# Optimization experiments

Hardware: AMD Instinct MI355X
Metric: run time of the kernel (lower is better)

The kernel has to match this reference:

```python
import jax, jax.numpy as jnp
import numpy as np

H = 1024          # hiddenSize
V = 50257         # outputSize (vocab)
L = 512           # maxLength (encoder length)


def setup_inputs() -> dict:
    key = jax.random.key(0)
    ks = jax.random.split(key, 16)
    s = 0.02
    return {
        "input": jax.random.randint(ks[0], (1,), 0, V),
        "hidden": jax.random.normal(ks[1], (1, 1, H), jnp.float32),
        "encoder_outputs": jax.random.normal(ks[2], (L, H), jnp.float32),
        "emb": jax.random.normal(ks[3], (V, H), jnp.float32) * s,
        "W_attn": jax.random.normal(ks[4], (L, 2 * H), jnp.float32) * s,
        "b_attn": jnp.zeros((L,), jnp.float32),
        "W_comb": jax.random.normal(ks[5], (H, 2 * H), jnp.float32) * s,
        "b_comb": jnp.zeros((H,), jnp.float32),
        "W_ih": jax.random.normal(ks[6], (3 * H, H), jnp.float32) * s,
        "W_hh": jax.random.normal(ks[7], (3 * H, H), jnp.float32) * s,
        "b_ih": jnp.zeros((3 * H,), jnp.float32),
        "b_hh": jnp.zeros((3 * H,), jnp.float32),
        "W_out": jax.random.normal(ks[8], (V, H), jnp.float32) * s,
        "b_out": jnp.zeros((V,), jnp.float32),
    }


def reference(input, hidden, encoder_outputs, emb, W_attn, b_attn,
              W_comb, b_comb, W_ih, W_hh, b_ih, b_hh, W_out, b_out):
    # embedding lookup: [1, H] (dropout p=0 -> identity)
    embedded = emb[input]
    h = hidden[0]                                   # [1, H]
    # attention over encoder positions
    attn_logits = jnp.concatenate([embedded, h], axis=1) @ W_attn.T + b_attn
    attn_weights = jax.nn.softmax(attn_logits, axis=1)      # [1, L]
    attn_applied = attn_weights @ encoder_outputs           # [1, H]
    # combine and relu
    x = jnp.concatenate([embedded, attn_applied], axis=1) @ W_comb.T + b_comb
    x = jax.nn.relu(x)                                      # [1, H]
    # single GRU step (PyTorch gate layout: r, z, n)
    gi = x @ W_ih.T + b_ih                                  # [1, 3H]
    gh = h @ W_hh.T + b_hh                                  # [1, 3H]
    i_r, i_z, i_n = jnp.split(gi, 3, axis=1)
    h_r, h_z, h_n = jnp.split(gh, 3, axis=1)
    r = jax.nn.sigmoid(i_r + h_r)
    z = jax.nn.sigmoid(i_z + h_z)
    n = jnp.tanh(i_n + r * h_n)
    h_new = (1.0 - z) * n + z * h                           # [1, H]
    # output distribution
    output = jax.nn.log_softmax(h_new @ W_out.T + b_out, axis=1)  # [1, V]
    return output, h_new[None], attn_weights
```

## Files before the change

kernel.cpp:

```cpp
#include <hip/hip_runtime.h>
#include <cmath>

#define H 1024
#define V 50257
#define L 512
#define NB5 1571
#define NPART 128

typedef float f4 __attribute__((ext_vector_type(4)));

__device__ __forceinline__ float wred_sum(float v) {
#pragma unroll
    for (int o = 32; o > 0; o >>= 1) v += __shfl_xor(v, o, 64);
    return v;
}
__device__ __forceinline__ float dot4f(f4 a, f4 b) {
    return a.x * b.x + a.y * b.y + a.z * b.z + a.w * b.w;
}
__device__ __forceinline__ void ms_merge(float& m, float& s, float m2, float s2) {
    float M = fmaxf(m, m2);
    if (M == -INFINITY) { m = M; s = 0.f; return; }
    s = s * expf(m - M) + s2 * expf(m2 - M);
    m = M;
}

__global__ void k_phase1(const int* __restrict__ tok,
                         const float* __restrict__ hid,
                         const float* __restrict__ emb,
                         const float* __restrict__ Wa,
                         const float* __restrict__ ba,
                         const float* __restrict__ enc,
                         const float* __restrict__ Whh,
                         const float* __restrict__ bhh,
                         float* __restrict__ elg,
                         float* __restrict__ pbuf,
                         float* __restrict__ gh) {
    const int t = threadIdx.x, lane = t & 63, wv = t >> 6, b = blockIdx.x;
    const f4* h4 = (const f4*)hid;
    if (b < NPART) {
        const int l = b * 4 + wv;
        const f4* e4 = (const f4*)(emb + (size_t)tok[0] * H);
        const f4* wr = (const f4*)(Wa + (size_t)l * 2048);
        float acc = 0.f;
#pragma unroll
        for (int k = 0; k < 8; ++k) {
            int f = 64 * k + lane;
            f4 s = (f < 256) ? e4[f] : h4[f - 256];
            acc += dot4f(wr[f], s);
        }
        acc = wred_sum(acc);
        __shared__ float se[4];
        const float e = expf(acc + ba[l]);
        if (lane == 0) { se[wv] = e; elg[l] = e; }
        __syncthreads();
        f4 a = {0.f, 0.f, 0.f, 0.f};
#pragma unroll
        for (int r = 0; r < 4; ++r)
            a += se[r] * ((const f4*)(enc + (size_t)(b * 4 + r) * H))[t];
        ((f4*)pbuf)[b * 256 + t] = a;
    } else {
        const int j = (b - NPART) * 4 + wv;
        const f4* wh = (const f4*)(Whh + (size_t)j * H);
        float acc = 0.f;
#pragma unroll
        for (int k = 0; k < 4; ++k) {
            int f = 64 * k + lane;
            acc += dot4f(wh[f], h4[f]);
        }
        acc = wred_sum(acc);
        if (lane == 0) gh[j] = acc + bhh[j];
    }
}

__global__ void k_reduce(const float* __restrict__ elg,
                         const float* __restrict__ pbuf,
                         float* __restrict__ aa,
                         float* __restrict__ wout) {
    const int t = threadIdx.x, b = blockIdx.x;
    const int g = t >> 6, c = t & 63;
    __shared__ float red[4];
    const float e0 = elg[t], e1 = elg[t + 256];
    float s = wred_sum(e0 + e1);
    if (c == 0) red[g] = s;
    __syncthreads();
    const float invS = 1.f / (red[0] + red[1] + red[2] + red[3]);
    const int col = b * 64 + c;
    f4 a = {0.f, 0.f, 0.f, 0.f};
#pragma unroll 8
    for (int i = g; i < NPART; i += 4) a += ((const f4*)pbuf)[i * 256 + col];
    __shared__ f4 racc[4][64];
    racc[g][c] = a;
    __syncthreads();
    if (g == 0) {
        f4 tot = (racc[0][c] + racc[1][c] + racc[2][c] + racc[3][c]) * invS;
        ((f4*)aa)[col] = tot;
    }
    if (b == 0) { wout[t] = e0 * invS; wout[t + 256] = e1 * invS; }
}

__global__ void k_comb(const int* __restrict__ tok,
                       const float* __restrict__ emb,
                       const float* __restrict__ aa,
                       const float* __restrict__ Wc,
                       const float* __restrict__ bcb,
                       float* __restrict__ xv) {
    const int lane = threadIdx.x & 63, wv = threadIdx.x >> 6;
    const int j = blockIdx.x * 4 + wv;
    const f4* e4 = (const f4*)(emb + (size_t)tok[0] * H);
    const f4* a4 = (const f4*)aa;
    const f4* wr = (const f4*)(Wc + (size_t)j * 2048);
    float acc = 0.f;
#pragma unroll
    for (int k = 0; k < 4; ++k) {
        int f = 64 * k + lane;
        acc += dot4f(wr[f], e4[f]);
        acc += dot4f(wr[256 + f], a4[f]);
    }
    acc = wred_sum(acc);
    if (lane == 0) xv[j] = fmaxf(acc + bcb[j], 0.f);
}

__global__ void k_gates_gru(const float* __restrict__ xv,
                            const float* __restrict__ hid,
                            const float* __restrict__ Wih,
                            const float* __restrict__ bih,
                            const float* __restrict__ gh,
                            float* __restrict__ hn_out,
                            float* __restrict__ hn_ws) {
    const int lane = threadIdx.x & 63, wv = threadIdx.x >> 6;
    const int j = blockIdx.x * 4 + wv;
    const f4* x4 = (const f4*)xv;
    f4 xreg[4];
#pragma unroll
    for (int k = 0; k < 4; ++k) xreg[k] = x4[64 * k + lane];
    float g[3];
#pragma unroll
    for (int p = 0; p < 3; ++p) {
        const f4* wr = (const f4*)(Wih + (size_t)(j + p * H) * H);
        float acc = 0.f;
#pragma unroll
        for (int k = 0; k < 4; ++k) acc += dot4f(wr[64 * k + lane], xreg[k]);
        g[p] = wred_sum(acc) + bih[j + p * H];
    }
    if (lane == 0) {
        float r = 1.f / (1.f + expf(-(g[0] + gh[j])));
        float z = 1.f / (1.f + expf(-(g[1] + gh[j + H])));
        float n = tanhf(g[2] + r * gh[j + 2 * H]);
        float hv = (1.f - z) * n + z * hid[j];
        hn_out[j] = hv;
        hn_ws[j] = hv;
    }
}

__global__ void k_out_gemv(const float* __restrict__ hn,
                           const float* __restrict__ Wo,
                           const float* __restrict__ bo,
                           float* __restrict__ logits,
                           float* __restrict__ pm,
                           float* __restrict__ ps) {
    const int lane = threadIdx.x & 63, wv = threadIdx.x >> 6;
    const int b = blockIdx.x;
    const int rbase = b * 32 + wv * 8;
    const f4* h4 = (const f4*)hn;
    f4 hreg[4];
#pragma unroll
    for (int k = 0; k < 4; ++k) hreg[k] = h4[64 * k + lane];
    float m = -INFINITY, s = 0.f;
    if (b != NB5 - 1) {
        float lv[8];
#pragma unroll
        for (int i = 0; i < 8; ++i) {
            const f4* wr = (const f4*)(Wo + (size_t)(rbase + i) * H);
            float acc = 0.f;
#pragma unroll
            for (int k = 0; k < 4; ++k)
                acc += dot4f(__builtin_nontemporal_load(wr + 64 * k + lane), hreg[k]);
            acc = wred_sum(acc) + bo[rbase + i];
            if (lane == 0) logits[rbase + i] = acc;
            lv[i] = acc;
        }
#pragma unroll
        for (int i = 0; i < 8; ++i) m = fmaxf(m, lv[i]);
#pragma unroll
        for (int i = 0; i < 8; ++i) s += expf(lv[i] - m);
    } else {
#pragma unroll
        for (int i = 0; i < 8; ++i) {
            const int v = rbase + i;
            if (v < V) {
                const f4* wr = (const f4*)(Wo + (size_t)v * H);
                float acc = 0.f;
#pragma unroll
                for (int k = 0; k < 4; ++k)
                    acc += dot4f(__builtin_nontemporal_load(wr + 64 * k + lane), hreg[k]);
                acc = wred_sum(acc) + bo[v];
                if (lane == 0) logits[v] = acc;
                float M = fmaxf(m, acc);
                s = s * expf(m - M) + expf(acc - M);
                m = M;
            }
        }
    }
    __shared__ float smm[4], sms[4];
    if (lane == 0) { smm[wv] = m; sms[wv] = s; }
    __syncthreads();
    if (threadIdx.x == 0) {
        float M = smm[0], S = sms[0];
#pragma unroll
        for (int i = 1; i < 4; ++i) ms_merge(M, S, smm[i], sms[i]);
        pm[b] = M; ps[b] = S;
    }
}

__global__ void k_finalize(float* __restrict__ out,
                           const float* __restrict__ pm,
                           const float* __restrict__ ps) {
    const int t = threadIdx.x, lane = t & 63, wv = t >> 6;
    float m = -INFINITY, s = 0.f;
    for (int i = t; i < NB5; i += 256) ms_merge(m, s, pm[i], ps[i]);
#pragma unroll
    for (int o = 32; o > 0; o >>= 1) {
        float m2 = __shfl_xor(m, o, 64);
        float s2 = __shfl_xor(s, o, 64);
        ms_merge(m, s, m2, s2);
    }
    __shared__ float smm[4], sms[4];
    __shared__ float Cs;
    if (lane == 0) { smm[wv] = m; sms[wv] = s; }
    __syncthreads();
    if (t == 0) {
        float M = smm[0], S = sms[0];
#pragma unroll
        for (int i = 1; i < 4; ++i) ms_merge(M, S, smm[i], sms[i]);
        Cs = M + logf(S);
    }
    __syncthreads();
    const float C = Cs;
    const int v = blockIdx.x * 256 + t;
    if (v < V) out[v] -= C;
}

extern "C" void kernel_launch(void* const* d_in, const int* in_sizes, int n_in,
                              void* d_out, int out_size, void* d_ws, size_t ws_size,
                              hipStream_t stream) {
    const int*   tok = (const int*)d_in[0];
    const float* hid = (const float*)d_in[1];
    const float* enc = (const float*)d_in[2];
    const float* emb = (const float*)d_in[3];
    const float* Wa  = (const float*)d_in[4];
    const float* ba  = (const float*)d_in[5];
    const float* Wc  = (const float*)d_in[6];
    const float* bc  = (const float*)d_in[7];
    const float* Wih = (const float*)d_in[8];
    const float* Whh = (const float*)d_in[9];
    const float* bih = (const float*)d_in[10];
    const float* bhh = (const float*)d_in[11];
    const float* Wo  = (const float*)d_in[12];
    const float* bo  = (const float*)d_in[13];

    float* out = (float*)d_out;
    float* ws  = (float*)d_ws;
    float* elg  = ws;
    float* gh   = ws + 512;
    float* aa   = ws + 3584;
    float* xv   = ws + 4608;
    float* hn   = ws + 5632;
    float* pm   = ws + 6656;
    float* psum = ws + 8256;
    float* pbuf = ws + 9856;

    float* out_logits = out;
    float* out_hnew   = out + V;
    float* out_attnw  = out + V + H;

    k_phase1<<<NPART + 768, 256, 0, stream>>>(tok, hid, emb, Wa, ba, enc, Whh, bhh,
                                              elg, pbuf, gh);
    k_reduce<<<4, 256, 0, stream>>>(elg, pbuf, aa, out_attnw);
    k_comb<<<256, 256, 0, stream>>>(tok, emb, aa, Wc, bc, xv);
    k_gates_gru<<<256, 256, 0, stream>>>(xv, hid, Wih, bih, gh, out_hnew, hn);
    k_out_gemv<<<NB5, 256, 0, stream>>>(hn, Wo, bo, out_logits, pm, psum);
    k_finalize<<<197, 256, 0, stream>>>(out_logits, pm, psum);
}
```

Measured before the change: 61.27 us.

## Rebalance work split across attention, reduce, and output GEMV kernels

The attention-score stage now uses 256 blocks, each handling two rows split into halves across waves, which doubles the partial buffer. The reduce kernel uses 16 blocks with 16 partial groups each. The output GEMV changes from 1571 blocks with 8 fixed rows per wave to a 1024-block grid-stride loop that uses an online max/sum and plain loads instead of nontemporal ones. The aim is better occupancy and load balance, at the cost of serial online-softmax dependencies and a loss of per-wave memory-level parallelism in the dominant GEMV.

```diff
diff --git a/kernel.cpp b/kernel.cpp
--- a/kernel.cpp
+++ b/kernel.cpp
@@ -4,8 +4,8 @@
 #define H 1024
 #define V 50257
 #define L 512
-#define NB5 1571
-#define NPART 128
+#define NBGEMV 1024
+#define NPART 256
 
 typedef float f4 __attribute__((ext_vector_type(4)));
 
@@ -38,25 +38,31 @@
     const int t = threadIdx.x, lane = t & 63, wv = t >> 6, b = blockIdx.x;
     const f4* h4 = (const f4*)hid;
     if (b < NPART) {
-        const int l = b * 4 + wv;
+        const int row = 2 * b + (wv >> 1);
+        const int half = wv & 1;
         const f4* e4 = (const f4*)(emb + (size_t)tok[0] * H);
-        const f4* wr = (const f4*)(Wa + (size_t)l * 2048);
-        float acc = 0.f;
-#pragma unroll
-        for (int k = 0; k < 8; ++k) {
-            int f = 64 * k + lane;
+        const f4* wr = (const f4*)(Wa + (size_t)row * 2048);
+        float acc = 0.f;
+#pragma unroll
+        for (int k = 0; k < 4; ++k) {
+            int f = half * 256 + 64 * k + lane;
             f4 s = (f < 256) ? e4[f] : h4[f - 256];
             acc += dot4f(wr[f], s);
         }
         acc = wred_sum(acc);
-        __shared__ float se[4];
-        const float e = expf(acc + ba[l]);
-        if (lane == 0) { se[wv] = e; elg[l] = e; }
+        __shared__ float sp[4];
+        __shared__ float se[2];
+        if (lane == 0) sp[wv] = acc;
         __syncthreads();
-        f4 a = {0.f, 0.f, 0.f, 0.f};
-#pragma unroll
-        for (int r = 0; r < 4; ++r)
-            a += se[r] * ((const f4*)(enc + (size_t)(b * 4 + r) * H))[t];
+        if (t == 0) {
+            float E0 = expf(sp[0] + sp[1] + ba[2 * b]);
+            float E1 = expf(sp[2] + sp[3] + ba[2 * b + 1]);
+            se[0] = E0; se[1] = E1;
+            elg[2 * b] = E0; elg[2 * b + 1] = E1;
+        }
+        __syncthreads();
+        f4 a = se[0] * ((const f4*)(enc + (size_t)(2 * b) * H))[t]
+             + se[1] * ((const f4*)(enc + (size_t)(2 * b + 1) * H))[t];
         ((f4*)pbuf)[b * 256 + t] = a;
     } else {
         const int j = (b - NPART) * 4 + wv;
@@ -77,23 +83,26 @@
                          float* __restrict__ aa,
                          float* __restrict__ wout) {
     const int t = threadIdx.x, b = blockIdx.x;
-    const int g = t >> 6, c = t & 63;
+    const int g = t >> 4, c = t & 15;
     __shared__ float red[4];
     const float e0 = elg[t], e1 = elg[t + 256];
     float s = wred_sum(e0 + e1);
-    if (c == 0) red[g] = s;
+    if ((t & 63) == 0) red[t >> 6] = s;
     __syncthreads();
     const float invS = 1.f / (red[0] + red[1] + red[2] + red[3]);
-    const int col = b * 64 + c;
+    const int col = b * 16 + c;
     f4 a = {0.f, 0.f, 0.f, 0.f};
-#pragma unroll 8
-    for (int i = g; i < NPART; i += 4) a += ((const f4*)pbuf)[i * 256 + col];
-    __shared__ f4 racc[4][64];
+#pragma unroll
+    for (int i = 0; i < 16; ++i)
+        a += ((const f4*)pbuf)[(size_t)(g + 16 * i) * 256 + col];
+    __shared__ f4 racc[16][16];
     racc[g][c] = a;
     __syncthreads();
     if (g == 0) {
-        f4 tot = (racc[0][c] + racc[1][c] + racc[2][c] + racc[3][c]) * invS;
-        ((f4*)aa)[col] = tot;
+        f4 tot = {0.f, 0.f, 0.f, 0.f};
+#pragma unroll
+        for (int i = 0; i < 16; ++i) tot += racc[i][c];
+        ((f4*)aa)[col] = tot * invS;
     }
     if (b == 0) { wout[t] = e0 * invS; wout[t + 256] = e1 * invS; }
 }
@@ -160,46 +169,22 @@
                            float* __restrict__ ps) {
     const int lane = threadIdx.x & 63, wv = threadIdx.x >> 6;
     const int b = blockIdx.x;
-    const int rbase = b * 32 + wv * 8;
+    const int gw = b * 4 + wv;
     const f4* h4 = (const f4*)hn;
     f4 hreg[4];
 #pragma unroll
     for (int k = 0; k < 4; ++k) hreg[k] = h4[64 * k + lane];
     float m = -INFINITY, s = 0.f;
-    if (b != NB5 - 1) {
-        float lv[8];
-#pragma unroll
-        for (int i = 0; i < 8; ++i) {
-            const f4* wr = (const f4*)(Wo + (size_t)(rbase + i) * H);
-            float acc = 0.f;
-#pragma unroll
-            for (int k = 0; k < 4; ++k)
-                acc += dot4f(__builtin_nontemporal_load(wr + 64 * k + lane), hreg[k]);
-            acc = wred_sum(acc) + bo[rbase + i];
-            if (lane == 0) logits[rbase + i] = acc;
-            lv[i] = acc;
-        }
-#pragma unroll
-        for (int i = 0; i < 8; ++i) m = fmaxf(m, lv[i]);
-#pragma unroll
-        for (int i = 0; i < 8; ++i) s += expf(lv[i] - m);
-    } else {
-#pragma unroll
-        for (int i = 0; i < 8; ++i) {
-            const int v = rbase + i;
-            if (v < V) {
-                const f4* wr = (const f4*)(Wo + (size_t)v * H);
-                float acc = 0.f;
-#pragma unroll
-                for (int k = 0; k < 4; ++k)
-                    acc += dot4f(__builtin_nontemporal_load(wr + 64 * k + lane), hreg[k]);
-                acc = wred_sum(acc) + bo[v];
-                if (lane == 0) logits[v] = acc;
-                float M = fmaxf(m, acc);
-                s = s * expf(m - M) + expf(acc - M);
-                m = M;
-            }
-        }
+    for (int v = gw; v < V; v += 4096) {
+        const f4* wr = (const f4*)(Wo + (size_t)v * H);
+        float acc = 0.f;
+#pragma unroll
+        for (int k = 0; k < 4; ++k) acc += dot4f(wr[64 * k + lane], hreg[k]);
+        acc = wred_sum(acc) + bo[v];
+        if (lane == 0) logits[v] = acc;
+        float M = fmaxf(m, acc);
+        s = s * expf(m - M) + expf(acc - M);
+        m = M;
     }
     __shared__ float smm[4], sms[4];
     if (lane == 0) { smm[wv] = m; sms[wv] = s; }
@@ -217,7 +202,7 @@
                            const float* __restrict__ ps) {
     const int t = threadIdx.x, lane = t & 63, wv = t >> 6;
     float m = -INFINITY, s = 0.f;
-    for (int i = t; i < NB5; i += 256) ms_merge(m, s, pm[i], ps[i]);
+    for (int i = t; i < NBGEMV; i += 256) ms_merge(m, s, pm[i], ps[i]);
 #pragma unroll
     for (int o = 32; o > 0; o >>= 1) {
         float m2 = __shfl_xor(m, o, 64);
@@ -266,8 +251,8 @@
     float* xv   = ws + 4608;
     float* hn   = ws + 5632;
     float* pm   = ws + 6656;
-    float* psum = ws + 8256;
-    float* pbuf = ws + 9856;
+    float* psum = ws + 7680;
+    float* pbuf = ws + 8704;
 
     float* out_logits = out;
     float* out_hnew   = out + V;
@@ -275,9 +260,9 @@
 
     k_phase1<<<NPART + 768, 256, 0, stream>>>(tok, hid, emb, Wa, ba, enc, Whh, bhh,
                                               elg, pbuf, gh);
-    k_reduce<<<4, 256, 0, stream>>>(elg, pbuf, aa, out_attnw);
+    k_reduce<<<16, 256, 0, stream>>>(elg, pbuf, aa, out_attnw);
     k_comb<<<256, 256, 0, stream>>>(tok, emb, aa, Wc, bc, xv);
     k_gates_gru<<<256, 256, 0, stream>>>(xv, hid, Wih, bih, gh, out_hnew, hn);
-    k_out_gemv<<<NB5, 256, 0, stream>>>(hn, Wo, bo, out_logits, pm, psum);
+    k_out_gemv<<<NBGEMV, 256, 0, stream>>>(hn, Wo, bo, out_logits, pm, psum);
     k_finalize<<<197, 256, 0, stream>>>(out_logits, pm, psum);
 }
```

Measured after the change: 55.71 us. 1.1x faster.
